# Performance work log

Measured on AMD Instinct MI355X. Metric: run time of the kernel, lower is better.

Reference implementation:

```python
import jax, jax.numpy as jnp
import numpy as np

BASE_TEMP = 0.07
CLASS_TEMPS = jnp.array([0.08, 0.05, 0.10], dtype=jnp.float32)  # idx 0,1,2
EPS = 1e-08


def setup_inputs() -> dict:
    key = jax.random.key(0)
    k1, k2 = jax.random.split(key)
    B, D = 8192, 128
    embeddings = jax.random.normal(k1, (B, D), dtype=jnp.float32)
    labels = jax.random.randint(k2, (B,), 0, 3, dtype=jnp.int64)
    return {"embeddings": embeddings, "labels": labels}


def reference(embeddings, labels):
    B = embeddings.shape[0]
    # per-row temperature from the row's class label
    temps = CLASS_TEMPS[labels]  # [B]
    sim = jnp.matmul(embeddings, embeddings.T)  # [B, B]
    logits = sim / temps[:, None]
    # subtract detached row max (stability, gradient-stopped as in .detach())
    logits = logits - jax.lax.stop_gradient(jnp.max(logits, axis=1, keepdims=True))
    # denominator includes the self term (original sums exp over all j)
    log_prob = logits - jnp.log(jnp.sum(jnp.exp(logits), axis=1, keepdims=True) + EPS)
    # positives: same label, excluding self
    pos_mask = (labels[:, None] == labels[None, :]).astype(jnp.float32)
    pos_mask = pos_mask * (1.0 - jnp.eye(B, dtype=jnp.float32))
    pos_count = jnp.sum(pos_mask, axis=1)  # [B]
    valid = pos_count > 0
    loss_i = -(BASE_TEMP / temps) * jnp.sum(pos_mask * log_prob, axis=1) / (pos_count + EPS)
    n_valid = jnp.sum(valid.astype(jnp.float32))
    total = jnp.sum(jnp.where(valid, loss_i, 0.0))
    return jnp.where(n_valid > 0, total / jnp.maximum(n_valid, 1.0), 0.0)
```

## Files before the change

kernel.cpp:

```cpp
#include <hip/hip_runtime.h>
#include <hip/hip_bf16.h>


#define B_ROWS 8192
#define D_DIM 128
#define NSPLIT 16
#define JRANGE (B_ROWS / NSPLIT)
#define NSTEPS (JRANGE / 32)
#define BASE_TEMP 0.07f
#define LOG2E 1.4426950408889634f
#define LN2 0.6931471805599453f
#define FIX_SCALE 1048576.0f

typedef __bf16 bf16x8 __attribute__((ext_vector_type(8)));
typedef __bf16 bf16x4 __attribute__((ext_vector_type(4)));
typedef float floatx16 __attribute__((ext_vector_type(16)));
typedef unsigned long long u64;

__device__ __forceinline__ float class_invtemp(int lbl) {
    return (lbl == 0) ? 12.5f : ((lbl == 1) ? 20.0f : 10.0f);
}

__device__ __forceinline__ u64 fix64(float v) {
    return (u64)(long long)llrintf(v * FIX_SCALE);
}

__device__ __forceinline__ void load_lds16(const __bf16* g, __bf16* l) {
    __builtin_amdgcn_global_load_lds(
        (const __attribute__((address_space(1))) void*)g,
        (__attribute__((address_space(3))) void*)l,
        16, 0, 0);
}

__global__ __launch_bounds__(256) void k0_prep(
        const float* __restrict__ E, const int* __restrict__ labels,
        __bf16* __restrict__ Ebf, __bf16* __restrict__ Ebs,
        float* __restrict__ nrm,
        float* __restrict__ Spart ,
        int* __restrict__ cntpart ) {
    const int blk = blockIdx.x;
    const int tid = threadIdx.x;
    const int row0 = blk * 32;

    __shared__ float4 red[3][256];
    __shared__ int scnt[3];
    if (tid < 3) scnt[tid] = 0;

    float4 cls0 = {0.f, 0.f, 0.f, 0.f};
    float4 cls1 = {0.f, 0.f, 0.f, 0.f};
    float4 cls2 = {0.f, 0.f, 0.f, 0.f};

    const float4* src = reinterpret_cast<const float4*>(E + (size_t)row0 * D_DIM);
    #pragma unroll
    for (int p = 0; p < 4; ++p) {
        int idx = p * 256 + tid;
        float4 v = src[idx];
        int r = idx >> 5, k4 = idx & 31;
        int R = row0 + r;
        int lab = labels[R];
        float sc = class_invtemp(lab) * LOG2E;
        int T = R >> 5;
        int l = (R & 31) + ((k4 >> 1) & 1) * 32;
        int c = k4 >> 2;
        size_t dst = (size_t)T * 4096 + c * 512 + l * 8 + (k4 & 1) * 4;
        bf16x4 o  = { (__bf16)v.x, (__bf16)v.y, (__bf16)v.z, (__bf16)v.w };
        bf16x4 os = { (__bf16)(v.x * sc), (__bf16)(v.y * sc),
                      (__bf16)(v.z * sc), (__bf16)(v.w * sc) };
        *reinterpret_cast<bf16x4*>(Ebf + dst) = o;
        *reinterpret_cast<bf16x4*>(Ebs + dst) = os;
        float s = v.x * v.x + v.y * v.y + v.z * v.z + v.w * v.w;
        s += __shfl_xor(s, 1);  s += __shfl_xor(s, 2);  s += __shfl_xor(s, 4);
        s += __shfl_xor(s, 8);  s += __shfl_xor(s, 16);
        if ((tid & 31) == 0) nrm[R] = s;
        if (lab == 0) { cls0.x += v.x; cls0.y += v.y; cls0.z += v.z; cls0.w += v.w; }
        else if (lab == 1) { cls1.x += v.x; cls1.y += v.y; cls1.z += v.z; cls1.w += v.w; }
        else { cls2.x += v.x; cls2.y += v.y; cls2.z += v.z; cls2.w += v.w; }
    }
    red[0][tid] = cls0;
    red[1][tid] = cls1;
    red[2][tid] = cls2;
    if (tid < 32) atomicAdd(&scnt[labels[row0 + tid]], 1);
    __syncthreads();

    if (tid < 128) {
        const int k4 = tid >> 2, comp = tid & 3;
        const float* rf = reinterpret_cast<const float*>(red);
        #pragma unroll
        for (int c = 0; c < 3; ++c) {
            float a = 0.f;
            #pragma unroll
            for (int w = 0; w < 8; ++w)
                a += rf[(c * 256 + k4 + 32 * w) * 4 + comp];
            Spart[((size_t)blk * 3 + c) * 128 + tid] = a;
        }
    }
    if (tid < 3) cntpart[blk * 4 + tid] = scnt[tid];
}

__global__ __launch_bounds__(256) void k2_stats(
        const __bf16* __restrict__ Ebf, const __bf16* __restrict__ Ebs,
        const int* __restrict__ labels, const float* __restrict__ nrm,
        float* __restrict__ part ,
        const float* __restrict__ Spart, const int* __restrict__ cntpart,
        float* __restrict__ S , float* __restrict__ counts ,
        u64* __restrict__ lossfix, u64* __restrict__ validfix,
        unsigned int* __restrict__ done) {
    __shared__ __bf16 Ab[2][4096];

    const int tid = threadIdx.x;
    const int lane = tid & 63;
    const int wave = tid >> 6;
    const int itile = blockIdx.x;
    const int split = blockIdx.y;
    const int col = lane & 31;
    const int icol = itile * 128 + wave * 32 + col;

    const float negm = -class_invtemp(labels[icol]) * LOG2E * nrm[icol];

    const int iT = itile * 4 + wave;
    const __bf16* bbase = Ebs + (size_t)iT * 4096 + lane * 8;
    bf16x8 Bf[8];
    #pragma unroll
    for (int c = 0; c < 8; ++c)
        Bf[c] = *reinterpret_cast<const bf16x8*>(bbase + c * 512);

    floatx16 init0;
    #pragma unroll
    for (int r = 0; r < 16; ++r) init0[r] = negm;

    const __bf16* abase = Ebf + (size_t)split * NSTEPS * 4096;
    const int woff = wave * 1024 + lane * 8;

    load_lds16(abase + woff,       &Ab[0][wave * 1024]);
    load_lds16(abase + woff + 512, &Ab[0][wave * 1024 + 512]);
    __syncthreads();

    float Zacc[4];
    #pragma unroll
    for (int q = 0; q < 4; ++q) Zacc[q] = 0.f;

    for (int s = 0; s < NSTEPS; ++s) {
        if (s + 1 < NSTEPS) {
            const __bf16* g = abase + (size_t)(s + 1) * 4096 + woff;
            __bf16* l = &Ab[(s + 1) & 1][wave * 1024];
            load_lds16(g, l);
            load_lds16(g + 512, l + 512);
        }

        const __bf16* abuf = &Ab[s & 1][0];
        bf16x8 A[8];
        #pragma unroll
        for (int c = 0; c < 8; ++c)
            A[c] = *reinterpret_cast<const bf16x8*>(abuf + c * 512 + lane * 8);

        floatx16 a1;
        #pragma unroll
        for (int r = 0; r < 16; ++r) a1[r] = 0.f;
        floatx16 a0 = __builtin_amdgcn_mfma_f32_32x32x16_bf16(A[0], Bf[0], init0, 0, 0, 0);
        a1 = __builtin_amdgcn_mfma_f32_32x32x16_bf16(A[4], Bf[4], a1, 0, 0, 0);
        a0 = __builtin_amdgcn_mfma_f32_32x32x16_bf16(A[1], Bf[1], a0, 0, 0, 0);
        a1 = __builtin_amdgcn_mfma_f32_32x32x16_bf16(A[5], Bf[5], a1, 0, 0, 0);
        a0 = __builtin_amdgcn_mfma_f32_32x32x16_bf16(A[2], Bf[2], a0, 0, 0, 0);
        a1 = __builtin_amdgcn_mfma_f32_32x32x16_bf16(A[6], Bf[6], a1, 0, 0, 0);
        a0 = __builtin_amdgcn_mfma_f32_32x32x16_bf16(A[3], Bf[3], a0, 0, 0, 0);
        a1 = __builtin_amdgcn_mfma_f32_32x32x16_bf16(A[7], Bf[7], a1, 0, 0, 0);

        #pragma unroll
        for (int q = 0; q < 4; ++q) {
            Zacc[q] += (__builtin_amdgcn_exp2f(a0[4 * q]     + a1[4 * q])
                      + __builtin_amdgcn_exp2f(a0[4 * q + 1] + a1[4 * q + 1]))
                     + (__builtin_amdgcn_exp2f(a0[4 * q + 2] + a1[4 * q + 2])
                      + __builtin_amdgcn_exp2f(a0[4 * q + 3] + a1[4 * q + 3]));
        }

        __syncthreads();
    }

    float Zt = (Zacc[0] + Zacc[1]) + (Zacc[2] + Zacc[3]);
    Zt += __shfl_xor(Zt, 32);
    if (lane < 32)
        part[(size_t)split * B_ROWS + icol] = Zt;

    if (split == 0) {
        if (itile < 3 && tid < 128) {
            float a = 0.f;
            #pragma unroll 8
            for (int g = 0; g < 256; ++g)
                a += Spart[((size_t)g * 3 + itile) * 128 + tid];
            S[itile * 128 + tid] = a;
        } else if (itile == 3 && tid < 3) {
            int a = 0;
            #pragma unroll 8
            for (int g = 0; g < 256; ++g) a += cntpart[g * 4 + tid];
            counts[tid] = (float)a;
        } else if (itile == 4 && tid == 0) {
            *lossfix = 0ull;
            *validfix = 0ull;
            *done = 0u;
        }
    }
}

__global__ __launch_bounds__(256) void k3_rowloss(
        const float* __restrict__ E, const int* __restrict__ labels,
        const float* __restrict__ S, const float* __restrict__ counts,
        const float* __restrict__ nrm, const float* __restrict__ part,
        u64* __restrict__ lossfix, u64* __restrict__ validfix,
        unsigned int* __restrict__ done, float* __restrict__ out) {
    __shared__ float sS[384];
    const int tid = threadIdx.x;
    if (tid < 128) {
        sS[tid]       = S[tid];
        sS[128 + tid] = S[128 + tid];
        sS[256 + tid] = S[256 + tid];
    }
    __syncthreads();

    const int r = tid >> 3, g = tid & 7;
    const int i = blockIdx.x * 32 + r;
    const int lab = labels[i];
    const float invt = class_invtemp(lab);

    const float4* er = reinterpret_cast<const float4*>(E + (size_t)i * D_DIM);
    const float4* sr = reinterpret_cast<const float4*>(&sS[lab * 128]);
    float dotS = 0.f;
    #pragma unroll
    for (int q = 0; q < 4; ++q) {
        float4 v = er[g * 4 + q];
        float4 s = sr[g * 4 + q];
        dotS += v.x * s.x + v.y * s.y + v.z * s.z + v.w * s.w;
    }
    float Zp = 0.f;
    #pragma unroll
    for (int p = 0; p < NSPLIT / 8; ++p)
        Zp += part[(size_t)(g + p * 8) * B_ROWS + i];

    #pragma unroll
    for (int off = 1; off < 8; off <<= 1) {
        dotS += __shfl_xor(dotS, off);
        Zp   += __shfl_xor(Zp, off);
    }

    float loss = 0.f;
    int valid = 0;
    if (g == 0) {
        const float nr = nrm[i];
        const float C = counts[lab] - 1.0f;
        const float lse = invt * nr + LN2 * __builtin_amdgcn_logf(Zp);
        const float P_nat = invt * (dotS - nr);
        if (C > 0.f) {
            loss = -(BASE_TEMP * invt) * (P_nat - C * lse) / (C + 1e-8f);
            valid = 1;
        }
    }
    loss += __shfl_down(loss, 8);   valid += __shfl_down(valid, 8);
    loss += __shfl_down(loss, 16);  valid += __shfl_down(valid, 16);
    loss += __shfl_down(loss, 32);  valid += __shfl_down(valid, 32);

    __shared__ float rl[4];
    __shared__ int rv[4];
    if ((tid & 63) == 0) { rl[tid >> 6] = loss; rv[tid >> 6] = valid; }
    __syncthreads();
    if (tid == 0) {
        float bt = (rl[0] + rl[1]) + (rl[2] + rl[3]);
        int bv = (rv[0] + rv[1]) + (rv[2] + rv[3]);
        atomicAdd(lossfix, fix64(bt));
        atomicAdd(validfix, (u64)bv);
        __threadfence();
        unsigned int t = atomicAdd(done, 1u);
        if (t == gridDim.x - 1) {
            u64 L = atomicAdd(lossfix, 0ull);
            u64 V = atomicAdd(validfix, 0ull);
            double T = (double)(long long)L * (1.0 / (double)FIX_SCALE);
            double N = (double)(long long)V;
            out[0] = (N > 0.0) ? (float)(T / fmax(N, 1.0)) : 0.f;
        }
    }
}

extern "C" void kernel_launch(void* const* d_in, const int* in_sizes, int n_in,
                              void* d_out, int out_size, void* d_ws, size_t ws_size,
                              hipStream_t stream) {
    const float* E = (const float*)d_in[0];
    const int* labels = (const int*)d_in[1];
    float* out = (float*)d_out;
    char* ws = (char*)d_ws;

    const size_t OFF_EBF   = 0;
    const size_t OFF_EBS   = (size_t)2 << 20;
    const size_t OFF_NRM   = (size_t)4 << 20;
    const size_t OFF_SPART = OFF_NRM + 32768;
    const size_t OFF_CNTP  = OFF_SPART + 393216;
    const size_t OFF_S     = OFF_CNTP + 4096;
    const size_t OFF_MISC  = OFF_S + 2048;
    const size_t OFF_PART  = (size_t)5 << 20;

    __bf16* Ebf = (__bf16*)(ws + OFF_EBF);
    __bf16* Ebs = (__bf16*)(ws + OFF_EBS);
    float* nrm = (float*)(ws + OFF_NRM);
    float* Spart = (float*)(ws + OFF_SPART);
    int* cntpart = (int*)(ws + OFF_CNTP);
    float* S = (float*)(ws + OFF_S);
    float* counts = (float*)(ws + OFF_MISC);
    u64* lossfix = (u64*)(ws + OFF_MISC + 16);
    u64* validfix = (u64*)(ws + OFF_MISC + 24);
    unsigned int* done = (unsigned int*)(ws + OFF_MISC + 32);
    float* part = (float*)(ws + OFF_PART);

    k0_prep<<<256, 256, 0, stream>>>(E, labels, Ebf, Ebs, nrm, Spart, cntpart);
    k2_stats<<<dim3(64, NSPLIT), 256, 0, stream>>>(
        Ebf, Ebs, labels, nrm, part, Spart, cntpart, S, counts,
        lossfix, validfix, done);
    k3_rowloss<<<256, 256, 0, stream>>>(E, labels, S, counts, nrm, part,
                                        lossfix, validfix, done, out);
}
```

Measured before the change: 47.48 us.

## Fuse row-loss kernel into stats kernel via last-block ticket workers

Removes the third kernel launch by having the last 32 blocks of the stats kernel (by atomic ticket) spin-wait until all blocks finish, then compute per-row losses and the final reduction. Zeroing of the counters moves into the prep kernel. It also staggers each block's starting step along the j dimension so concurrent blocks read different A tiles. The cost is a spin-wait in late blocks and a row-loss phase that runs on only 32 blocks with one row per thread and strided row reads.

```diff
diff --git a/kernel.cpp b/kernel.cpp
--- a/kernel.cpp
+++ b/kernel.cpp
@@ -7,6 +7,8 @@
 #define NSPLIT 16
 #define JRANGE (B_ROWS / NSPLIT)
 #define NSTEPS (JRANGE / 32)
+#define NBLOCKS (64 * NSPLIT)
+#define NWORKERS 32
 #define BASE_TEMP 0.07f
 #define LOG2E 1.4426950408889634f
 #define LN2 0.6931471805599453f
@@ -37,10 +39,13 @@
         __bf16* __restrict__ Ebf, __bf16* __restrict__ Ebs,
         float* __restrict__ nrm,
         float* __restrict__ Spart ,
-        int* __restrict__ cntpart ) {
+        int* __restrict__ cntpart ,
+        u64* __restrict__ zeroblk ) {
     const int blk = blockIdx.x;
     const int tid = threadIdx.x;
     const int row0 = blk * 32;
+
+    if (blk == 0 && tid < 4) zeroblk[tid] = 0ull;
 
     __shared__ float4 red[3][256];
     __shared__ int scnt[3];
@@ -98,14 +103,20 @@
 }
 
 __global__ __launch_bounds__(256) void k2_stats(
+        const float* __restrict__ E,
         const __bf16* __restrict__ Ebf, const __bf16* __restrict__ Ebs,
         const int* __restrict__ labels, const float* __restrict__ nrm,
         float* __restrict__ part ,
         const float* __restrict__ Spart, const int* __restrict__ cntpart,
         float* __restrict__ S , float* __restrict__ counts ,
         u64* __restrict__ lossfix, u64* __restrict__ validfix,
-        unsigned int* __restrict__ done) {
+        unsigned int* __restrict__ done, unsigned int* __restrict__ done2,
+        float* __restrict__ out) {
     __shared__ __bf16 Ab[2][4096];
+    __shared__ float sS[384];
+    __shared__ float rl[4];
+    __shared__ int rv[4];
+    __shared__ unsigned int tkt;
 
     const int tid = threadIdx.x;
     const int lane = tid & 63;
@@ -130,24 +141,26 @@
 
     const __bf16* abase = Ebf + (size_t)split * NSTEPS * 4096;
     const int woff = wave * 1024 + lane * 8;
-
-    load_lds16(abase + woff,       &Ab[0][wave * 1024]);
-    load_lds16(abase + woff + 512, &Ab[0][wave * 1024 + 512]);
+    const int s0 = (itile * 5 + split * 3) & (NSTEPS - 1);
+
+    load_lds16(abase + (size_t)s0 * 4096 + woff,       &Ab[0][wave * 1024]);
+    load_lds16(abase + (size_t)s0 * 4096 + woff + 512, &Ab[0][wave * 1024 + 512]);
     __syncthreads();
 
     float Zacc[4];
     #pragma unroll
     for (int q = 0; q < 4; ++q) Zacc[q] = 0.f;
 
-    for (int s = 0; s < NSTEPS; ++s) {
-        if (s + 1 < NSTEPS) {
-            const __bf16* g = abase + (size_t)(s + 1) * 4096 + woff;
-            __bf16* l = &Ab[(s + 1) & 1][wave * 1024];
+    for (int q = 0; q < NSTEPS; ++q) {
+        if (q + 1 < NSTEPS) {
+            const int sn = (s0 + q + 1) & (NSTEPS - 1);
+            const __bf16* g = abase + (size_t)sn * 4096 + woff;
+            __bf16* l = &Ab[(q + 1) & 1][wave * 1024];
             load_lds16(g, l);
             load_lds16(g + 512, l + 512);
         }
 
-        const __bf16* abuf = &Ab[s & 1][0];
+        const __bf16* abuf = &Ab[q & 1][0];
         bf16x8 A[8];
         #pragma unroll
         for (int c = 0; c < 8; ++c)
@@ -166,13 +179,12 @@
         a1 = __builtin_amdgcn_mfma_f32_32x32x16_bf16(A[7], Bf[7], a1, 0, 0, 0);
 
         #pragma unroll
-        for (int q = 0; q < 4; ++q) {
-            Zacc[q] += (__builtin_amdgcn_exp2f(a0[4 * q]     + a1[4 * q])
-                      + __builtin_amdgcn_exp2f(a0[4 * q + 1] + a1[4 * q + 1]))
-                     + (__builtin_amdgcn_exp2f(a0[4 * q + 2] + a1[4 * q + 2])
-                      + __builtin_amdgcn_exp2f(a0[4 * q + 3] + a1[4 * q + 3]));
-        }
-
+        for (int p = 0; p < 4; ++p) {
+            Zacc[p] += (__builtin_amdgcn_exp2f(a0[4 * p]     + a1[4 * p])
+                      + __builtin_amdgcn_exp2f(a0[4 * p + 1] + a1[4 * p + 1]))
+                     + (__builtin_amdgcn_exp2f(a0[4 * p + 2] + a1[4 * p + 2])
+                      + __builtin_amdgcn_exp2f(a0[4 * p + 3] + a1[4 * p + 3]));
+        }
         __syncthreads();
     }
 
@@ -193,22 +205,19 @@
             #pragma unroll 8
             for (int g = 0; g < 256; ++g) a += cntpart[g * 4 + tid];
             counts[tid] = (float)a;
-        } else if (itile == 4 && tid == 0) {
-            *lossfix = 0ull;
-            *validfix = 0ull;
-            *done = 0u;
-        }
-    }
-}
-
-__global__ __launch_bounds__(256) void k3_rowloss(
-        const float* __restrict__ E, const int* __restrict__ labels,
-        const float* __restrict__ S, const float* __restrict__ counts,
-        const float* __restrict__ nrm, const float* __restrict__ part,
-        u64* __restrict__ lossfix, u64* __restrict__ validfix,
-        unsigned int* __restrict__ done, float* __restrict__ out) {
-    __shared__ float sS[384];
-    const int tid = threadIdx.x;
+        }
+    }
+
+    __threadfence();
+    if (tid == 0) tkt = atomicAdd(done, 1u);
+    __syncthreads();
+    const unsigned int t = tkt;
+    if (t < NBLOCKS - NWORKERS) return;
+    const int w = t - (NBLOCKS - NWORKERS);
+
+    if (tid == 0) { while (atomicAdd(done, 0u) < NBLOCKS) { __builtin_amdgcn_s_sleep(8); } }
+    __syncthreads();
+
     if (tid < 128) {
         sS[tid]       = S[tid];
         sS[128 + tid] = S[128 + tid];
@@ -216,49 +225,38 @@
     }
     __syncthreads();
 
-    const int r = tid >> 3, g = tid & 7;
-    const int i = blockIdx.x * 32 + r;
-    const int lab = labels[i];
-    const float invt = class_invtemp(lab);
-
+    const int i = w * 256 + tid;
+    const int lab2 = labels[i];
+    const float invt = class_invtemp(lab2);
     const float4* er = reinterpret_cast<const float4*>(E + (size_t)i * D_DIM);
-    const float4* sr = reinterpret_cast<const float4*>(&sS[lab * 128]);
+    const float4* sr = reinterpret_cast<const float4*>(&sS[lab2 * 128]);
     float dotS = 0.f;
     #pragma unroll
-    for (int q = 0; q < 4; ++q) {
-        float4 v = er[g * 4 + q];
-        float4 s = sr[g * 4 + q];
+    for (int k4 = 0; k4 < 32; ++k4) {
+        float4 v = er[k4];
+        float4 s = sr[k4];
         dotS += v.x * s.x + v.y * s.y + v.z * s.z + v.w * s.w;
     }
     float Zp = 0.f;
     #pragma unroll
-    for (int p = 0; p < NSPLIT / 8; ++p)
-        Zp += part[(size_t)(g + p * 8) * B_ROWS + i];
-
-    #pragma unroll
-    for (int off = 1; off < 8; off <<= 1) {
-        dotS += __shfl_xor(dotS, off);
-        Zp   += __shfl_xor(Zp, off);
-    }
-
+    for (int p = 0; p < NSPLIT; ++p)
+        Zp += part[(size_t)p * B_ROWS + i];
+
+    const float nr = nrm[i];
+    const float C = counts[lab2] - 1.0f;
+    const float lse = invt * nr + LN2 * __builtin_amdgcn_logf(Zp);
+    const float P_nat = invt * (dotS - nr);
     float loss = 0.f;
     int valid = 0;
-    if (g == 0) {
-        const float nr = nrm[i];
-        const float C = counts[lab] - 1.0f;
-        const float lse = invt * nr + LN2 * __builtin_amdgcn_logf(Zp);
-        const float P_nat = invt * (dotS - nr);
-        if (C > 0.f) {
-            loss = -(BASE_TEMP * invt) * (P_nat - C * lse) / (C + 1e-8f);
-            valid = 1;
-        }
-    }
-    loss += __shfl_down(loss, 8);   valid += __shfl_down(valid, 8);
-    loss += __shfl_down(loss, 16);  valid += __shfl_down(valid, 16);
-    loss += __shfl_down(loss, 32);  valid += __shfl_down(valid, 32);
-
-    __shared__ float rl[4];
-    __shared__ int rv[4];
+    if (C > 0.f) {
+        loss = -(BASE_TEMP * invt) * (P_nat - C * lse) / (C + 1e-8f);
+        valid = 1;
+    }
+    #pragma unroll
+    for (int off = 32; off; off >>= 1) {
+        loss += __shfl_down(loss, off);
+        valid += __shfl_down(valid, off);
+    }
     if ((tid & 63) == 0) { rl[tid >> 6] = loss; rv[tid >> 6] = valid; }
     __syncthreads();
     if (tid == 0) {
@@ -267,8 +265,8 @@
         atomicAdd(lossfix, fix64(bt));
         atomicAdd(validfix, (u64)bv);
         __threadfence();
-        unsigned int t = atomicAdd(done, 1u);
-        if (t == gridDim.x - 1) {
+        unsigned int t2 = atomicAdd(done2, 1u);
+        if (t2 == NWORKERS - 1) {
             u64 L = atomicAdd(lossfix, 0ull);
             u64 V = atomicAdd(validfix, 0ull);
             double T = (double)(long long)L * (1.0 / (double)FIX_SCALE);
@@ -302,15 +300,16 @@
     int* cntpart = (int*)(ws + OFF_CNTP);
     float* S = (float*)(ws + OFF_S);
     float* counts = (float*)(ws + OFF_MISC);
-    u64* lossfix = (u64*)(ws + OFF_MISC + 16);
-    u64* validfix = (u64*)(ws + OFF_MISC + 24);
-    unsigned int* done = (unsigned int*)(ws + OFF_MISC + 32);
+    u64* zeroblk = (u64*)(ws + OFF_MISC + 32);
+    u64* lossfix = zeroblk;
+    u64* validfix = zeroblk + 1;
+    unsigned int* done = (unsigned int*)(zeroblk + 2);
+    unsigned int* done2 = (unsigned int*)(zeroblk + 3);
     float* part = (float*)(ws + OFF_PART);
 
-    k0_prep<<<256, 256, 0, stream>>>(E, labels, Ebf, Ebs, nrm, Spart, cntpart);
+    k0_prep<<<256, 256, 0, stream>>>(E, labels, Ebf, Ebs, nrm, Spart, cntpart,
+                                     zeroblk);
     k2_stats<<<dim3(64, NSPLIT), 256, 0, stream>>>(
-        Ebf, Ebs, labels, nrm, part, Spart, cntpart, S, counts,
-        lossfix, validfix, done);
-    k3_rowloss<<<256, 256, 0, stream>>>(E, labels, S, counts, nrm, part,
-                                        lossfix, validfix, done, out);
-}
+        E, Ebf, Ebs, labels, nrm, part, Spart, cntpart, S, counts,
+        lossfix, validfix, done, done2, out);
+}
```

Result: slower. 114.9 us (+142.0%).

## Register-block two column tiles per wave in k2_stats to reuse LDS A fragments

Applied to the files above, without the earlier changes.

Each wave now holds B fragments for two 32-column tiles and feeds every A fragment read from LDS into two MFMAs, halving LDS traffic per MFMA. To keep the same block count, the i-dimension grid is halved and NSPLIT is doubled, so each block walks a shorter j range. The row-max bias is now added before the exp instead of being folded into the MFMA init, and the launch bounds ask for 4 blocks per CU. The cost is higher VGPR pressure, which may force spills under the occupancy hint, and more partial sums for k3 to reduce.

```diff
diff --git a/kernel.cpp b/kernel.cpp
--- a/kernel.cpp
+++ b/kernel.cpp
@@ -4,7 +4,7 @@
 
 #define B_ROWS 8192
 #define D_DIM 128
-#define NSPLIT 16
+#define NSPLIT 32
 #define JRANGE (B_ROWS / NSPLIT)
 #define NSTEPS (JRANGE / 32)
 #define BASE_TEMP 0.07f
@@ -97,7 +97,7 @@
     if (tid < 3) cntpart[blk * 4 + tid] = scnt[tid];
 }
 
-__global__ __launch_bounds__(256) void k2_stats(
+__global__ __launch_bounds__(256, 4) void k2_stats(
         const __bf16* __restrict__ Ebf, const __bf16* __restrict__ Ebs,
         const int* __restrict__ labels, const float* __restrict__ nrm,
         float* __restrict__ part ,
@@ -113,20 +113,20 @@
     const int itile = blockIdx.x;
     const int split = blockIdx.y;
     const int col = lane & 31;
-    const int icol = itile * 128 + wave * 32 + col;
-
-    const float negm = -class_invtemp(labels[icol]) * LOG2E * nrm[icol];
-
-    const int iT = itile * 4 + wave;
-    const __bf16* bbase = Ebs + (size_t)iT * 4096 + lane * 8;
-    bf16x8 Bf[8];
-    #pragma unroll
-    for (int c = 0; c < 8; ++c)
-        Bf[c] = *reinterpret_cast<const bf16x8*>(bbase + c * 512);
-
-    floatx16 init0;
-    #pragma unroll
-    for (int r = 0; r < 16; ++r) init0[r] = negm;
+    const int icol0 = itile * 256 + wave * 64 + col;
+    const int icol1 = icol0 + 32;
+
+    const float negm0 = -class_invtemp(labels[icol0]) * LOG2E * nrm[icol0];
+    const float negm1 = -class_invtemp(labels[icol1]) * LOG2E * nrm[icol1];
+
+    const int iT0 = itile * 8 + wave * 2;
+    const __bf16* b0 = Ebs + (size_t)iT0 * 4096 + lane * 8;
+    bf16x8 Bf0[8], Bf1[8];
+    #pragma unroll
+    for (int c = 0; c < 8; ++c) {
+        Bf0[c] = *reinterpret_cast<const bf16x8*>(b0 + c * 512);
+        Bf1[c] = *reinterpret_cast<const bf16x8*>(b0 + 4096 + c * 512);
+    }
 
     const __bf16* abase = Ebf + (size_t)split * NSTEPS * 4096;
     const int woff = wave * 1024 + lane * 8;
@@ -135,9 +135,9 @@
     load_lds16(abase + woff + 512, &Ab[0][wave * 1024 + 512]);
     __syncthreads();
 
-    float Zacc[4];
-    #pragma unroll
-    for (int q = 0; q < 4; ++q) Zacc[q] = 0.f;
+    float Zacc0[4], Zacc1[4];
+    #pragma unroll
+    for (int q = 0; q < 4; ++q) { Zacc0[q] = 0.f; Zacc1[q] = 0.f; }
 
     for (int s = 0; s < NSTEPS; ++s) {
         if (s + 1 < NSTEPS) {
@@ -148,38 +148,56 @@
         }
 
         const __bf16* abuf = &Ab[s & 1][0];
-        bf16x8 A[8];
+        floatx16 a0, a1;
         #pragma unroll
-        for (int c = 0; c < 8; ++c)
-            A[c] = *reinterpret_cast<const bf16x8*>(abuf + c * 512 + lane * 8);
-
-        floatx16 a1;
-        #pragma unroll
-        for (int r = 0; r < 16; ++r) a1[r] = 0.f;
-        floatx16 a0 = __builtin_amdgcn_mfma_f32_32x32x16_bf16(A[0], Bf[0], init0, 0, 0, 0);
-        a1 = __builtin_amdgcn_mfma_f32_32x32x16_bf16(A[4], Bf[4], a1, 0, 0, 0);
-        a0 = __builtin_amdgcn_mfma_f32_32x32x16_bf16(A[1], Bf[1], a0, 0, 0, 0);
-        a1 = __builtin_amdgcn_mfma_f32_32x32x16_bf16(A[5], Bf[5], a1, 0, 0, 0);
-        a0 = __builtin_amdgcn_mfma_f32_32x32x16_bf16(A[2], Bf[2], a0, 0, 0, 0);
-        a1 = __builtin_amdgcn_mfma_f32_32x32x16_bf16(A[6], Bf[6], a1, 0, 0, 0);
-        a0 = __builtin_amdgcn_mfma_f32_32x32x16_bf16(A[3], Bf[3], a0, 0, 0, 0);
-        a1 = __builtin_amdgcn_mfma_f32_32x32x16_bf16(A[7], Bf[7], a1, 0, 0, 0);
+        for (int r = 0; r < 16; ++r) { a0[r] = 0.f; a1[r] = 0.f; }
+
+        {
+            bf16x8 A[4];
+            #pragma unroll
+            for (int c = 0; c < 4; ++c)
+                A[c] = *reinterpret_cast<const bf16x8*>(abuf + c * 512 + lane * 8);
+            #pragma unroll
+            for (int c = 0; c < 4; ++c) {
+                a0 = __builtin_amdgcn_mfma_f32_32x32x16_bf16(A[c], Bf0[c], a0, 0, 0, 0);
+                a1 = __builtin_amdgcn_mfma_f32_32x32x16_bf16(A[c], Bf1[c], a1, 0, 0, 0);
+            }
+        }
+        {
+            bf16x8 A[4];
+            #pragma unroll
+            for (int c = 0; c < 4; ++c)
+                A[c] = *reinterpret_cast<const bf16x8*>(abuf + (c + 4) * 512 + lane * 8);
+            #pragma unroll
+            for (int c = 0; c < 4; ++c) {
+                a0 = __builtin_amdgcn_mfma_f32_32x32x16_bf16(A[c], Bf0[c + 4], a0, 0, 0, 0);
+                a1 = __builtin_amdgcn_mfma_f32_32x32x16_bf16(A[c], Bf1[c + 4], a1, 0, 0, 0);
+            }
+        }
 
         #pragma unroll
         for (int q = 0; q < 4; ++q) {
-            Zacc[q] += (__builtin_amdgcn_exp2f(a0[4 * q]     + a1[4 * q])
-                      + __builtin_amdgcn_exp2f(a0[4 * q + 1] + a1[4 * q + 1]))
-                     + (__builtin_amdgcn_exp2f(a0[4 * q + 2] + a1[4 * q + 2])
-                      + __builtin_amdgcn_exp2f(a0[4 * q + 3] + a1[4 * q + 3]));
+            Zacc0[q] += (__builtin_amdgcn_exp2f(a0[4 * q]     + negm0)
+                       + __builtin_amdgcn_exp2f(a0[4 * q + 1] + negm0))
+                      + (__builtin_amdgcn_exp2f(a0[4 * q + 2] + negm0)
+                       + __builtin_amdgcn_exp2f(a0[4 * q + 3] + negm0));
+            Zacc1[q] += (__builtin_amdgcn_exp2f(a1[4 * q]     + negm1)
+                       + __builtin_amdgcn_exp2f(a1[4 * q + 1] + negm1))
+                      + (__builtin_amdgcn_exp2f(a1[4 * q + 2] + negm1)
+                       + __builtin_amdgcn_exp2f(a1[4 * q + 3] + negm1));
         }
 
         __syncthreads();
     }
 
-    float Zt = (Zacc[0] + Zacc[1]) + (Zacc[2] + Zacc[3]);
-    Zt += __shfl_xor(Zt, 32);
-    if (lane < 32)
-        part[(size_t)split * B_ROWS + icol] = Zt;
+    float Zt0 = (Zacc0[0] + Zacc0[1]) + (Zacc0[2] + Zacc0[3]);
+    float Zt1 = (Zacc1[0] + Zacc1[1]) + (Zacc1[2] + Zacc1[3]);
+    Zt0 += __shfl_xor(Zt0, 32);
+    Zt1 += __shfl_xor(Zt1, 32);
+    if (lane < 32) {
+        part[(size_t)split * B_ROWS + icol0] = Zt0;
+        part[(size_t)split * B_ROWS + icol1] = Zt1;
+    }
 
     if (split == 0) {
         if (itile < 3 && tid < 128) {
@@ -308,7 +326,7 @@
     float* part = (float*)(ws + OFF_PART);
 
     k0_prep<<<256, 256, 0, stream>>>(E, labels, Ebf, Ebs, nrm, Spart, cntpart);
-    k2_stats<<<dim3(64, NSPLIT), 256, 0, stream>>>(
+    k2_stats<<<dim3(32, NSPLIT), 256, 0, stream>>>(
         Ebf, Ebs, labels, nrm, part, Spart, cntpart, S, counts,
         lossfix, validfix, done);
     k3_rowloss<<<256, 256, 0, stream>>>(E, labels, S, counts, nrm, part,
```

Result: slower. 72.96 us (+53.7%).
